# Performance work log

Hardware: AMD Instinct MI355X
Metric: run time of the kernel (lower is better)

The kernel has to match this reference:

```python
import jax, jax.numpy as jnp
import numpy as np

N, E, B = 16384, 65536, 32
D_IN, ED, H, L = 4, 5, 64, 3  # node feat, edge feat, hidden=output, num layers
NEG_SLOPE = 0.1
EPS = 1e-5


def _leaky(v):
    return jnp.where(v > 0, v, NEG_SLOPE * v)


def setup_inputs() -> dict:
    key = jax.random.key(0)
    ks = jax.random.split(key, 32)
    s = 0.05
    inp = {
        'x': jax.random.normal(ks[0], (N, D_IN), jnp.float32),
        'edge_index': jax.random.randint(ks[1], (2, E), 0, N),
        'edge_attr': jax.random.normal(ks[2], (E, ED), jnp.float32),
        'batch': jnp.sort(jax.random.randint(ks[3], (N,), 0, B)),
        # input projection Linear(4 -> H)
        'W_in': s * jax.random.normal(ks[4], (H, D_IN), jnp.float32),
        'b_in': jnp.zeros((H,), jnp.float32),
        # per-layer edge MLP: Linear(ED->H), Linear(H->H), Linear(H->H*H); stacked over L
        'ew1': s * jax.random.normal(ks[5], (L, H, ED), jnp.float32),
        'eb1': jnp.zeros((L, H), jnp.float32),
        'ew2': s * jax.random.normal(ks[6], (L, H, H), jnp.float32),
        'eb2': jnp.zeros((L, H), jnp.float32),
        'ew3': s * jax.random.normal(ks[7], (L, H * H, H), jnp.float32),
        'eb3': jnp.zeros((L, H * H), jnp.float32),
        # NNConv root weight + bias per layer
        'root_w': s * jax.random.normal(ks[8], (L, H, H), jnp.float32),
        'root_b': jnp.zeros((L, H), jnp.float32),
        # LayerNorm per layer
        'ln_g': jnp.ones((L, H), jnp.float32),
        'ln_b': jnp.zeros((L, H), jnp.float32),
        # prediction head: Linear(H->H), Linear(H->H//2), Linear(H//2->1)
        'pw1': s * jax.random.normal(ks[9], (H, H), jnp.float32),
        'pb1': jnp.zeros((H,), jnp.float32),
        'pw2': s * jax.random.normal(ks[10], (H // 2, H), jnp.float32),
        'pb2': jnp.zeros((H // 2,), jnp.float32),
        'pw3': s * jax.random.normal(ks[11], (1, H // 2), jnp.float32),
        'pb3': jnp.zeros((1,), jnp.float32),
    }
    return inp


def reference(x, edge_index, edge_attr, batch, W_in, b_in, ew1, eb1, ew2, eb2,
              ew3, eb3, root_w, root_b, ln_g, ln_b, pw1, pb1, pw2, pb2, pw3, pb3):
    src, dst = edge_index[0], edge_index[1]
    n_nodes = x.shape[0]
    n_edges = edge_attr.shape[0]
    # in-degree for scatter-mean (PyG yields 0 for isolated nodes)
    deg = jax.ops.segment_sum(jnp.ones((n_edges,), x.dtype), dst, num_segments=n_nodes)
    deg = jnp.maximum(deg, 1.0)[:, None]

    # input projection (dropout = identity in eval)
    h = _leaky(x @ W_in.T + b_in)

    for l in range(L):
        # edge MLP -> per-edge weight matrix [E, H, H]
        e = _leaky(edge_attr @ ew1[l].T + eb1[l])
        e = _leaky(e @ ew2[l].T + eb2[l])
        Wf = (e @ ew3[l].T + eb3[l]).reshape(n_edges, H, H)
        # message = x_src @ W_edge, scatter-mean to dst
        msg = jnp.einsum('ei,eio->eo', h[src], Wf)
        agg = jax.ops.segment_sum(msg, dst, num_segments=n_nodes) / deg
        out = agg + h @ root_w[l].T + root_b[l]
        # LayerNorm (post-norm)
        mu = out.mean(-1, keepdims=True)
        var = ((out - mu) ** 2).mean(-1, keepdims=True)
        out = (out - mu) * jax.lax.rsqrt(var + EPS) * ln_g[l] + ln_b[l]
        # activation + (identity) dropout + residual (in==out for all layers)
        h = _leaky(out) + h

    # global mean pool over graphs
    pooled = jax.ops.segment_sum(h, batch, num_segments=B)
    cnt = jax.ops.segment_sum(jnp.ones((n_nodes,), h.dtype), batch, num_segments=B)
    pooled = pooled / jnp.maximum(cnt, 1.0)[:, None]

    # prediction head
    p = _leaky(pooled @ pw1.T + pb1)
    p = _leaky(p @ pw2.T + pb2)
    pred = (p @ pw3.T + pb3).squeeze(-1)  # [B]
    return pred
```

## Files before the change

kernel.cpp:

```cpp
#include <hip/hip_runtime.h>
#include <hip/hip_bf16.h>

#define N_NODES 16384
#define N_EDGES 65536
#define NB      32
#define H       64
#define NLAYERS 3
#define NEG     0.1f
#define LN_EPS  1e-5f

typedef _Float16 f16;
typedef _Float16 f16x2 __attribute__((ext_vector_type(2)));
typedef _Float16 f16x8 __attribute__((ext_vector_type(8)));
typedef __fp16   hf16x2 __attribute__((ext_vector_type(2)));
typedef float    f32x16 __attribute__((ext_vector_type(16)));

union F16x8 { f16x8 v; f16x2 p[4]; int4 i4; int2 i2[2]; };
union F16x2U { f16x2 h2; hf16x2 raw; unsigned int u; };
union F16U   { f16 h; unsigned short u; };

__device__ __forceinline__ f16x2 pkrtz(float a, float b) {
    F16x2U t; t.raw = __builtin_amdgcn_cvt_pkrtz(a, b); return t.h2;
}
__device__ __forceinline__ float leaky(float v) { return v > 0.f ? v : NEG * v; }

__global__ __launch_bounds__(256) void k_setup(const float* __restrict__ x,
                                               const float* __restrict__ Win,
                                               const float* __restrict__ bin,
                                               const int* __restrict__ dst,
                                               const float* __restrict__ ew3,
                                               const float* __restrict__ eb3,
                                               float* __restrict__ h,
                                               float* __restrict__ deg,
                                               f16* __restrict__ Bp) {
    int bid = blockIdx.x;
    if (bid < 4096) {
        int t = bid * 256 + threadIdx.x;
        int n = t >> 6, j = t & 63;
        const float* xr = x + n * 4;
        const float* wr = Win + j * 4;
        float v = bin[j] + xr[0] * wr[0] + xr[1] * wr[1] + xr[2] * wr[2] + xr[3] * wr[3];
        h[t] = leaky(v);
    } else if (bid < 4352) {
        int e = (bid - 4096) * 256 + threadIdx.x;
        atomicAdd(&deg[dst[e]], 1.0f);
    } else {
        int tg    = (bid - 4352) * 256 + threadIdx.x;
        int lane  = tg & 63;
        int gslot = tg >> 6;
        int l     = gslot / 520;
        int slot  = gslot - l * 520;
        const float* ew3l = ew3 + (size_t)l * 262144;
        const float* eb3l = eb3 + (size_t)l * 4096;
        int i   = slot >> 3;
        int rem = slot & 7;
        int ks  = rem >> 1;
        int oq  = rem & 1;
        int o   = oq * 32 + (lane & 31);
        int k0  = ks * 16 + (lane >> 5) * 8;
        float v[8];
        if (i < 64) {
            const float* s = ew3l + ((size_t)(i * 64 + o)) * 64 + k0;
            float4 a = ((const float4*)s)[0];
            float4 b = ((const float4*)s)[1];
            v[0] = a.x; v[1] = a.y; v[2] = a.z; v[3] = a.w;
            v[4] = b.x; v[5] = b.y; v[6] = b.z; v[7] = b.w;
        } else {
#pragma unroll
            for (int j = 0; j < 8; j++) v[j] = eb3l[(k0 + j) * 64 + o];
        }
        union { int4 i4; f16 a[8]; } out;
#pragma unroll
        for (int j = 0; j < 8; j++) out.a[j] = (f16)v[j];
        *(int4*)(Bp + (size_t)l * 266240 + (size_t)slot * 512 + lane * 8) = out.i4;
    }
}

#define HS_STRIDE 76

__device__ __forceinline__ void loadB8(const f16* __restrict__ Bp, int c, int oq, int lane, F16x8* dstB) {
    const f16* base = Bp + (((size_t)(c * 16 + oq)) << 9) + lane * 8;
#pragma unroll
    for (int di = 0; di < 2; di++)
#pragma unroll
        for (int ks = 0; ks < 4; ks++)
            dstB[di * 4 + ks].i4 = *(const int4*)(base + ((di * 8 + ks * 2) << 9));
}
__device__ __forceinline__ void loadB4(const f16* __restrict__ Bp, int oq, int lane, F16x8* dstB) {
    const f16* base = Bp + (((size_t)(512 + oq)) << 9) + lane * 8;
#pragma unroll
    for (int ks = 0; ks < 4; ks++)
        dstB[ks].i4 = *(const int4*)(base + ((ks * 2) << 9));
}

__device__ __forceinline__ void msg_chunk2(int c, const F16x8* __restrict__ B,
                                           const unsigned short* hp0,
                                           const unsigned short* hp1,
                                           const f16x2 (*e2p)[4][4], f32x16* CC) {
    unsigned int rr0 = *(const unsigned int*)(hp0 + 2 * c);
    unsigned int rr1 = *(const unsigned int*)(hp1 + 2 * c);
    F16x2U h00, h01, h10, h11;
    h00.u = __builtin_amdgcn_perm(rr0, rr0, 0x01000100u);
    h10.u = __builtin_amdgcn_perm(rr0, rr0, 0x03020302u);
    h01.u = __builtin_amdgcn_perm(rr1, rr1, 0x01000100u);
    h11.u = __builtin_amdgcn_perm(rr1, rr1, 0x03020302u);
#pragma unroll
    for (int ks = 0; ks < 4; ks++) {
        F16x8 A00, A01, A10, A11;
#pragma unroll
        for (int r = 0; r < 4; r++) {
            A00.p[r] = h00.h2 * e2p[0][ks][r];
            A01.p[r] = h01.h2 * e2p[1][ks][r];
            A10.p[r] = h10.h2 * e2p[0][ks][r];
            A11.p[r] = h11.h2 * e2p[1][ks][r];
        }
        CC[0] = __builtin_amdgcn_mfma_f32_32x32x16_f16(A00.v, B[0 * 4 + ks].v, CC[0], 0, 0, 0);
        CC[1] = __builtin_amdgcn_mfma_f32_32x32x16_f16(A01.v, B[0 * 4 + ks].v, CC[1], 0, 0, 0);
        CC[2] = __builtin_amdgcn_mfma_f32_32x32x16_f16(A10.v, B[1 * 4 + ks].v, CC[2], 0, 0, 0);
        CC[3] = __builtin_amdgcn_mfma_f32_32x32x16_f16(A11.v, B[1 * 4 + ks].v, CC[3], 0, 0, 0);
    }
}

__global__ __launch_bounds__(256, 2) void k_msg(const float* __restrict__ h,
                                                const float* __restrict__ ea,
                                                const float* __restrict__ w1,
                                                const float* __restrict__ b1,
                                                const float* __restrict__ w2,
                                                const float* __restrict__ b2,
                                                const f16* __restrict__ Bp,
                                                const int* __restrict__ src,
                                                const int* __restrict__ dst,
                                                float* __restrict__ agg) {
    __shared__ __align__(16) unsigned short hsL[128 * HS_STRIDE];
    __shared__ __align__(16) unsigned short e1L[128 * 72];
    __shared__ __align__(16) unsigned short e2L[128 * 72];
    __shared__ float eas[128 * 8];
    __shared__ int dstL[128];

    const int t    = threadIdx.x;
    const int lane = t & 63;
    const int w    = t >> 6;
    const int eh   = w >> 1, oq = w & 1;
    const int m    = lane & 31;
    const int kp   = lane >> 5;
    const int eb   = blockIdx.x * 128;

    for (int idx = t; idx < 640; idx += 256) {
        int r = idx / 5, d = idx - r * 5;
        eas[r * 8 + d] = ea[(size_t)eb * 5 + idx];
    }
    {
        int e    = t >> 1;
        int half = t & 1;
        int nsrc = src[eb + e];
        const float4* hr = (const float4*)(h + (size_t)nsrc * 64 + half * 32);
        unsigned int* hrow = (unsigned int*)hsL + e * (HS_STRIDE / 2) + half * 16;
#pragma unroll
        for (int q = 0; q < 8; q++) {
            float4 v = hr[q];
            F16x2U p0, p1;
            p0.raw = __builtin_amdgcn_cvt_pkrtz(v.x, v.y);
            p1.raw = __builtin_amdgcn_cvt_pkrtz(v.z, v.w);
            hrow[q * 2 + 0] = p0.u;
            hrow[q * 2 + 1] = p1.u;
        }
        if (t < 128) dstL[t] = dst[eb + t];
    }
    __syncthreads();

    {
        int kk = t & 63;
        int eg = t >> 6;
        float w1r[5];
#pragma unroll
        for (int d = 0; d < 5; d++) w1r[d] = w1[kk * 5 + d];
        float b1r = b1[kk];
#pragma unroll 4
        for (int g = 0; g < 32; g++) {
            int row = eg * 32 + g;
            float4 a4 = *(const float4*)(eas + row * 8);
            float a5 = eas[row * 8 + 4];
            float v = b1r + a4.x * w1r[0] + a4.y * w1r[1] + a4.z * w1r[2] + a4.w * w1r[3] + a5 * w1r[4];
            F16U z; z.h = (f16)leaky(v);
            e1L[row * 72 + kk] = z.u;
        }
    }
    __syncthreads();

    {
        F16x8 W2f[4];
#pragma unroll
        for (int ks = 0; ks < 4; ks++) {
            const float* s = w2 + (size_t)(oq * 32 + m) * 64 + ks * 16 + kp * 8;
            float4 a = ((const float4*)s)[0];
            float4 b = ((const float4*)s)[1];
            W2f[ks].p[0] = pkrtz(a.x, a.y);
            W2f[ks].p[1] = pkrtz(a.z, a.w);
            W2f[ks].p[2] = pkrtz(b.x, b.y);
            W2f[ks].p[3] = pkrtz(b.z, b.w);
        }
        float b2r = b2[oq * 32 + m];
#pragma unroll
        for (int tt = 0; tt < 2; tt++) {
            f32x16 C2 = {0,0,0,0,0,0,0,0,0,0,0,0,0,0,0,0};
#pragma unroll
            for (int ks = 0; ks < 4; ks++) {
                F16x8 A;
                A.i4 = *(const int4*)(e1L + (size_t)((eh * 2 + tt) * 32 + m) * 72 + ks * 16 + kp * 8);
                C2 = __builtin_amdgcn_mfma_f32_32x32x16_f16(A.v, W2f[ks].v, C2, 0, 0, 0);
            }
#pragma unroll
            for (int reg = 0; reg < 16; reg++) {
                int r = (reg & 3) + 8 * (reg >> 2) + 4 * kp;
                F16U z; z.h = (f16)leaky(C2[reg] + b2r);
                e2L[((eh * 2 + tt) * 32 + r) * 72 + oq * 32 + m] = z.u;
            }
        }
    }
    __syncthreads();

    f16x2 e2p[2][4][4];
#pragma unroll
    for (int tt = 0; tt < 2; tt++) {
#pragma unroll
        for (int ks = 0; ks < 4; ks++) {
            F16x8 q;
            q.i4 = *(const int4*)(e2L + (size_t)((eh * 2 + tt) * 32 + m) * 72 + ks * 16 + kp * 8);
            e2p[tt][ks][0] = q.p[0]; e2p[tt][ks][1] = q.p[1];
            e2p[tt][ks][2] = q.p[2]; e2p[tt][ks][3] = q.p[3];
        }
    }

    f32x16 CC[4];
#pragma unroll
    for (int q = 0; q < 4; q++)
#pragma unroll
        for (int r = 0; r < 16; r++) CC[q][r] = 0.f;

    const unsigned short* hp0 = hsL + ((eh * 2 + 0) * 32 + m) * HS_STRIDE;
    const unsigned short* hp1 = hsL + ((eh * 2 + 1) * 32 + m) * HS_STRIDE;

    F16x8 B0[8], B1[8];
    loadB8(Bp, 0, oq, lane, B0);
    loadB8(Bp, 1, oq, lane, B1);
    for (int it = 0; it < 15; it++) {
        int c = it * 2;
        msg_chunk2(c,     B0, hp0, hp1, e2p, CC);  loadB8(Bp, c + 2, oq, lane, B0);
        msg_chunk2(c + 1, B1, hp0, hp1, e2p, CC);  loadB8(Bp, c + 3, oq, lane, B1);
    }
    msg_chunk2(30, B0, hp0, hp1, e2p, CC);
    loadB4(Bp, oq, lane, B0);
    msg_chunk2(31, B1, hp0, hp1, e2p, CC);

#pragma unroll
    for (int ks = 0; ks < 4; ks++) {
        int koff = (ks * 16 + kp * 8) * 2;
        const char* r0p = (const char*)hsL + (size_t)((eh * 2 + 0) * 32 + m) * (HS_STRIDE * 2) + koff;
        const char* r1p = (const char*)hsL + (size_t)((eh * 2 + 1) * 32 + m) * (HS_STRIDE * 2) + koff;
        F16x8 A0, A1;
        A0.i2[0] = *(const int2*)(r0p); A0.i2[1] = *(const int2*)(r0p + 8);
        A1.i2[0] = *(const int2*)(r1p); A1.i2[1] = *(const int2*)(r1p + 8);
        CC[0] = __builtin_amdgcn_mfma_f32_32x32x16_f16(A0.v, B0[ks].v, CC[0], 0, 0, 0);
        CC[1] = __builtin_amdgcn_mfma_f32_32x32x16_f16(A1.v, B0[ks].v, CC[1], 0, 0, 0);
    }

    int o = oq * 32 + m;
#pragma unroll
    for (int reg = 0; reg < 16; reg++) {
        int r = (reg & 3) + 8 * (reg >> 2) + 4 * kp;
        atomicAdd(&agg[(size_t)dstL[(eh * 2 + 0) * 32 + r] * 64 + o], CC[0][reg] + CC[2][reg]);
    }
#pragma unroll
    for (int reg = 0; reg < 16; reg++) {
        int r = (reg & 3) + 8 * (reg >> 2) + 4 * kp;
        atomicAdd(&agg[(size_t)dstL[(eh * 2 + 1) * 32 + r] * 64 + o], CC[1][reg] + CC[3][reg]);
    }
}

__global__ __launch_bounds__(256) void k_node(const float* __restrict__ agg,
                                              const float* __restrict__ deg,
                                              const float* __restrict__ rw,
                                              const float* __restrict__ rb,
                                              const float* __restrict__ lg,
                                              const float* __restrict__ lb,
                                              float* __restrict__ h,
                                              const int* __restrict__ batch,
                                              float* __restrict__ pooled,
                                              int last) {
    __shared__ __align__(16) unsigned short hA[64 * 72];
    __shared__ float outL[64][68];
    int t = threadIdx.x;
    int nb = blockIdx.x * 64;
    int lane = t & 63, w = t >> 6;
    int nq = w >> 1, oq = w & 1;
    int m = lane & 31, kp = lane >> 5;

    {
        int r = t >> 2, c0 = (t & 3) * 16;
        const float4* hr = (const float4*)(h + (size_t)(nb + r) * 64 + c0);
        unsigned int* drow = (unsigned int*)hA + r * 36 + c0 / 2;
#pragma unroll
        for (int q = 0; q < 4; q++) {
            float4 v = hr[q];
            F16x2U p0, p1;
            p0.raw = __builtin_amdgcn_cvt_pkrtz(v.x, v.y);
            p1.raw = __builtin_amdgcn_cvt_pkrtz(v.z, v.w);
            drow[q * 2] = p0.u; drow[q * 2 + 1] = p1.u;
        }
    }
    F16x8 Bf[4];
#pragma unroll
    for (int ks = 0; ks < 4; ks++) {
        const float* s = rw + (size_t)(oq * 32 + m) * 64 + ks * 16 + kp * 8;
        float4 a = ((const float4*)s)[0];
        float4 b = ((const float4*)s)[1];
        Bf[ks].p[0] = pkrtz(a.x, a.y);
        Bf[ks].p[1] = pkrtz(a.z, a.w);
        Bf[ks].p[2] = pkrtz(b.x, b.y);
        Bf[ks].p[3] = pkrtz(b.z, b.w);
    }
    __syncthreads();

    f32x16 C = {0,0,0,0,0,0,0,0,0,0,0,0,0,0,0,0};
#pragma unroll
    for (int ks = 0; ks < 4; ks++) {
        F16x8 A;
        A.i4 = *(const int4*)(hA + (size_t)(nq * 32 + m) * 72 + ks * 16 + kp * 8);
        C = __builtin_amdgcn_mfma_f32_32x32x16_f16(A.v, Bf[ks].v, C, 0, 0, 0);
    }

    int o = oq * 32 + m;
#pragma unroll
    for (int reg = 0; reg < 16; reg++) {
        int r = (reg & 3) + 8 * (reg >> 2) + 4 * kp;
        int n = nq * 32 + r;
        outL[n][o] = C[reg] + rb[o] + agg[(size_t)(nb + n) * 64 + o] / fmaxf(deg[nb + n], 1.0f);
    }
    __syncthreads();

    float gj = lg[lane], bj = lb[lane];
    float accp = 0.f;
    int cur = batch[nb + w * 16];
    for (int q = 0; q < 16; q++) {
        int n = w * 16 + q;
        float v = outL[n][lane];
        float mu = v;
#pragma unroll
        for (int msk = 32; msk > 0; msk >>= 1) mu += __shfl_xor(mu, msk);
        mu *= (1.f / 64.f);
        float d = v - mu;
        float var = d * d;
#pragma unroll
        for (int msk = 32; msk > 0; msk >>= 1) var += __shfl_xor(var, msk);
        var *= (1.f / 64.f);
        float ov = d * rsqrtf(var + LN_EPS) * gj + bj;
        float hn = leaky(ov) + h[(size_t)(nb + n) * 64 + lane];
        h[(size_t)(nb + n) * 64 + lane] = hn;
        if (last) {
            int b = batch[nb + n];
            if (b != cur) { atomicAdd(&pooled[cur * 64 + lane], accp); accp = 0.f; cur = b; }
            accp += hn;
        }
    }
    if (last) atomicAdd(&pooled[cur * 64 + lane], accp);
}

__global__ __launch_bounds__(256) void k_head(const float* __restrict__ pooled,
                                              const int* __restrict__ batch,
                                              const float* __restrict__ pw1, const float* __restrict__ pb1,
                                              const float* __restrict__ pw2, const float* __restrict__ pb2,
                                              const float* __restrict__ pw3, const float* __restrict__ pb3,
                                              float* __restrict__ out) {
    __shared__ float cntL[32];
    __shared__ float ps[32][64];
    __shared__ float p1[32][64];
    __shared__ float p2[32][32];
    int t = threadIdx.x;
    if (t < 32) cntL[t] = 0.f;
    __syncthreads();
    {
        const int4* bp4 = (const int4*)(batch + t * 64);
        int cur = batch[t * 64];
        float c = 0.f;
        for (int q = 0; q < 16; q++) {
            int4 b4 = bp4[q];
            int bs[4] = { b4.x, b4.y, b4.z, b4.w };
#pragma unroll
            for (int e = 0; e < 4; e++) {
                if (bs[e] != cur) { atomicAdd(&cntL[cur], c); cur = bs[e]; c = 0.f; }
                c += 1.f;
            }
        }
        atomicAdd(&cntL[cur], c);
    }
    __syncthreads();
    for (int idx = t; idx < 2048; idx += 256) {
        int b = idx >> 6, j = idx & 63;
        ps[b][j] = pooled[idx] / fmaxf(cntL[b], 1.0f);
    }
    __syncthreads();
    for (int idx = t; idx < 2048; idx += 256) {
        int b = idx >> 6, j = idx & 63;
        float v = pb1[j];
#pragma unroll 8
        for (int i = 0; i < 64; i++) v += ps[b][i] * pw1[j * 64 + i];
        p1[b][j] = leaky(v);
    }
    __syncthreads();
    for (int idx = t; idx < 1024; idx += 256) {
        int b = idx >> 5, j = idx & 31;
        float v = pb2[j];
#pragma unroll 8
        for (int i = 0; i < 64; i++) v += p1[b][i] * pw2[j * 64 + i];
        p2[b][j] = leaky(v);
    }
    __syncthreads();
    if (t < 32) {
        float v = pb3[0];
#pragma unroll 8
        for (int i = 0; i < 32; i++) v += p2[t][i] * pw3[i];
        out[t] = v;
    }
}

extern "C" void kernel_launch(void* const* d_in, const int* in_sizes, int n_in,
                              void* d_out, int out_size, void* d_ws, size_t ws_size,
                              hipStream_t stream) {
    const float* x    = (const float*)d_in[0];
    const int*   eidx = (const int*)  d_in[1];
    const float* ea   = (const float*)d_in[2];
    const int*   bat  = (const int*)  d_in[3];
    const float* Win  = (const float*)d_in[4];
    const float* bin  = (const float*)d_in[5];
    const float* ew1  = (const float*)d_in[6];
    const float* eb1  = (const float*)d_in[7];
    const float* ew2  = (const float*)d_in[8];
    const float* eb2  = (const float*)d_in[9];
    const float* ew3  = (const float*)d_in[10];
    const float* eb3  = (const float*)d_in[11];
    const float* rw   = (const float*)d_in[12];
    const float* rb   = (const float*)d_in[13];
    const float* lg   = (const float*)d_in[14];
    const float* lb   = (const float*)d_in[15];
    const float* pw1  = (const float*)d_in[16];
    const float* pb1  = (const float*)d_in[17];
    const float* pw2  = (const float*)d_in[18];
    const float* pb2  = (const float*)d_in[19];
    const float* pw3  = (const float*)d_in[20];
    const float* pb3  = (const float*)d_in[21];
    float* out = (float*)d_out;

    float* ws     = (float*)d_ws;
    float* h      = ws;
    float* agg    = ws + 1048576;
    float* deg    = ws + 4194304;
    float* pooled = ws + 4210688;
    f16*   Bp     = (f16*)(ws + 4212800);

    const int* srcp = eidx;
    const int* dstp = eidx + N_EDGES;

    (void)hipMemsetAsync(agg, 0, (size_t)3164224 * sizeof(float), stream);

    k_setup<<<4742, 256, 0, stream>>>(x, Win, bin, dstp, ew3, eb3, h, deg, Bp);

    for (int l = 0; l < NLAYERS; l++) {
        float* agg_l = agg + (size_t)l * N_NODES * H;
        k_msg <<<N_EDGES / 128, 256, 0, stream>>>(h, ea, ew1 + l * 320, eb1 + l * 64,
                                                  ew2 + l * 4096, eb2 + l * 64,
                                                  Bp + (size_t)l * 266240,
                                                  srcp, dstp, agg_l);
        k_node<<<N_NODES / 64, 256, 0, stream>>>(agg_l, deg, rw + l * 4096, rb + l * 64,
                                                 lg + l * 64, lb + l * 64, h,
                                                 bat, pooled, l == NLAYERS - 1 ? 1 : 0);
    }

    k_head<<<1, 256, 0, stream>>>(pooled, bat, pw1, pb1, pw2, pb2, pw3, pb3, out);
}
```

Measured before the change: 323.1 us.

## Remap message MFMA so each wave owns one edge tile and all outputs

The work split across the four waves of the message kernel changes. Before, each wave handled two 32-edge tiles for one half of the output columns. Now each wave handles one 32-edge tile for all 64 output columns, so each A operand (h times e2) is built once and reused across two B tiles. This halves the per-wave register copy of e2 and the VALU work spent forming A fragments. In exchange each wave loads twice as many B fragments per chunk (16 vs 8 int4 loads), which raises per-wave global/L2 traffic for the packed weight matrix and increases VGPR pressure for the B double buffer.

```diff
diff --git a/kernel.cpp b/kernel.cpp
--- a/kernel.cpp
+++ b/kernel.cpp
@@ -78,46 +78,38 @@
 
 #define HS_STRIDE 76
 
-__device__ __forceinline__ void loadB8(const f16* __restrict__ Bp, int c, int oq, int lane, F16x8* dstB) {
-    const f16* base = Bp + (((size_t)(c * 16 + oq)) << 9) + lane * 8;
-#pragma unroll
-    for (int di = 0; di < 2; di++)
-#pragma unroll
-        for (int ks = 0; ks < 4; ks++)
-            dstB[di * 4 + ks].i4 = *(const int4*)(base + ((di * 8 + ks * 2) << 9));
-}
-__device__ __forceinline__ void loadB4(const f16* __restrict__ Bp, int oq, int lane, F16x8* dstB) {
-    const f16* base = Bp + (((size_t)(512 + oq)) << 9) + lane * 8;
-#pragma unroll
-    for (int ks = 0; ks < 4; ks++)
-        dstB[ks].i4 = *(const int4*)(base + ((ks * 2) << 9));
-}
-
-__device__ __forceinline__ void msg_chunk2(int c, const F16x8* __restrict__ B,
-                                           const unsigned short* hp0,
-                                           const unsigned short* hp1,
-                                           const f16x2 (*e2p)[4][4], f32x16* CC) {
-    unsigned int rr0 = *(const unsigned int*)(hp0 + 2 * c);
-    unsigned int rr1 = *(const unsigned int*)(hp1 + 2 * c);
-    F16x2U h00, h01, h10, h11;
-    h00.u = __builtin_amdgcn_perm(rr0, rr0, 0x01000100u);
-    h10.u = __builtin_amdgcn_perm(rr0, rr0, 0x03020302u);
-    h01.u = __builtin_amdgcn_perm(rr1, rr1, 0x01000100u);
-    h11.u = __builtin_amdgcn_perm(rr1, rr1, 0x03020302u);
+__device__ __forceinline__ void loadB16(const f16* __restrict__ Bp, int c, int lane, F16x8* dstB) {
+    const f16* base = Bp + (((size_t)(c * 16)) << 9) + lane * 8;
+#pragma unroll
+    for (int s = 0; s < 16; s++)
+        dstB[s].i4 = *(const int4*)(base + (s << 9));
+}
+__device__ __forceinline__ void loadBias8(const f16* __restrict__ Bp, int lane, F16x8* dstB) {
+    const f16* base = Bp + (((size_t)512) << 9) + lane * 8;
+#pragma unroll
+    for (int s = 0; s < 8; s++)
+        dstB[s].i4 = *(const int4*)(base + (s << 9));
+}
+
+__device__ __forceinline__ void msg_chunk(int c, const F16x8* __restrict__ B,
+                                          const unsigned short* hp,
+                                          const f16x2 (*e2p)[4], f32x16* CC) {
+    unsigned int rr = *(const unsigned int*)(hp + 2 * c);
+    F16x2U h0, h1;
+    h0.u = __builtin_amdgcn_perm(rr, rr, 0x01000100u);
+    h1.u = __builtin_amdgcn_perm(rr, rr, 0x03020302u);
 #pragma unroll
     for (int ks = 0; ks < 4; ks++) {
-        F16x8 A00, A01, A10, A11;
+        F16x8 A0, A1;
 #pragma unroll
         for (int r = 0; r < 4; r++) {
-            A00.p[r] = h00.h2 * e2p[0][ks][r];
-            A01.p[r] = h01.h2 * e2p[1][ks][r];
-            A10.p[r] = h10.h2 * e2p[0][ks][r];
-            A11.p[r] = h11.h2 * e2p[1][ks][r];
-        }
-        CC[0] = __builtin_amdgcn_mfma_f32_32x32x16_f16(A00.v, B[0 * 4 + ks].v, CC[0], 0, 0, 0);
-        CC[1] = __builtin_amdgcn_mfma_f32_32x32x16_f16(A01.v, B[0 * 4 + ks].v, CC[1], 0, 0, 0);
-        CC[2] = __builtin_amdgcn_mfma_f32_32x32x16_f16(A10.v, B[1 * 4 + ks].v, CC[2], 0, 0, 0);
-        CC[3] = __builtin_amdgcn_mfma_f32_32x32x16_f16(A11.v, B[1 * 4 + ks].v, CC[3], 0, 0, 0);
+            A0.p[r] = h0.h2 * e2p[ks][r];
+            A1.p[r] = h1.h2 * e2p[ks][r];
+        }
+        CC[0] = __builtin_amdgcn_mfma_f32_32x32x16_f16(A0.v, B[ks * 2 + 0].v, CC[0], 0, 0, 0);
+        CC[1] = __builtin_amdgcn_mfma_f32_32x32x16_f16(A0.v, B[ks * 2 + 1].v, CC[1], 0, 0, 0);
+        CC[2] = __builtin_amdgcn_mfma_f32_32x32x16_f16(A1.v, B[8 + ks * 2 + 0].v, CC[2], 0, 0, 0);
+        CC[3] = __builtin_amdgcn_mfma_f32_32x32x16_f16(A1.v, B[8 + ks * 2 + 1].v, CC[3], 0, 0, 0);
     }
 }
 
@@ -219,16 +211,14 @@
     }
     __syncthreads();
 
-    f16x2 e2p[2][4][4];
-#pragma unroll
-    for (int tt = 0; tt < 2; tt++) {
-#pragma unroll
-        for (int ks = 0; ks < 4; ks++) {
-            F16x8 q;
-            q.i4 = *(const int4*)(e2L + (size_t)((eh * 2 + tt) * 32 + m) * 72 + ks * 16 + kp * 8);
-            e2p[tt][ks][0] = q.p[0]; e2p[tt][ks][1] = q.p[1];
-            e2p[tt][ks][2] = q.p[2]; e2p[tt][ks][3] = q.p[3];
-        }
+    const int tt = w;
+    f16x2 e2p[4][4];
+#pragma unroll
+    for (int ks = 0; ks < 4; ks++) {
+        F16x8 q;
+        q.i4 = *(const int4*)(e2L + (size_t)(tt * 32 + m) * 72 + ks * 16 + kp * 8);
+        e2p[ks][0] = q.p[0]; e2p[ks][1] = q.p[1];
+        e2p[ks][2] = q.p[2]; e2p[ks][3] = q.p[3];
     }
 
     f32x16 CC[4];
@@ -237,43 +227,36 @@
 #pragma unroll
         for (int r = 0; r < 16; r++) CC[q][r] = 0.f;
 
-    const unsigned short* hp0 = hsL + ((eh * 2 + 0) * 32 + m) * HS_STRIDE;
-    const unsigned short* hp1 = hsL + ((eh * 2 + 1) * 32 + m) * HS_STRIDE;
-
-    F16x8 B0[8], B1[8];
-    loadB8(Bp, 0, oq, lane, B0);
-    loadB8(Bp, 1, oq, lane, B1);
+    const unsigned short* hp = hsL + (tt * 32 + m) * HS_STRIDE;
+
+    F16x8 B0[16], B1[16];
+    loadB16(Bp, 0, lane, B0);
+    loadB16(Bp, 1, lane, B1);
     for (int it = 0; it < 15; it++) {
         int c = it * 2;
-        msg_chunk2(c,     B0, hp0, hp1, e2p, CC);  loadB8(Bp, c + 2, oq, lane, B0);
-        msg_chunk2(c + 1, B1, hp0, hp1, e2p, CC);  loadB8(Bp, c + 3, oq, lane, B1);
-    }
-    msg_chunk2(30, B0, hp0, hp1, e2p, CC);
-    loadB4(Bp, oq, lane, B0);
-    msg_chunk2(31, B1, hp0, hp1, e2p, CC);
+        msg_chunk(c,     B0, hp, e2p, CC);  loadB16(Bp, c + 2, lane, B0);
+        msg_chunk(c + 1, B1, hp, e2p, CC);  loadB16(Bp, c + 3, lane, B1);
+    }
+    msg_chunk(30, B0, hp, e2p, CC);
+    loadBias8(Bp, lane, B0);
+    msg_chunk(31, B1, hp, e2p, CC);
 
 #pragma unroll
     for (int ks = 0; ks < 4; ks++) {
         int koff = (ks * 16 + kp * 8) * 2;
-        const char* r0p = (const char*)hsL + (size_t)((eh * 2 + 0) * 32 + m) * (HS_STRIDE * 2) + koff;
-        const char* r1p = (const char*)hsL + (size_t)((eh * 2 + 1) * 32 + m) * (HS_STRIDE * 2) + koff;
-        F16x8 A0, A1;
-        A0.i2[0] = *(const int2*)(r0p); A0.i2[1] = *(const int2*)(r0p + 8);
-        A1.i2[0] = *(const int2*)(r1p); A1.i2[1] = *(const int2*)(r1p + 8);
-        CC[0] = __builtin_amdgcn_mfma_f32_32x32x16_f16(A0.v, B0[ks].v, CC[0], 0, 0, 0);
-        CC[1] = __builtin_amdgcn_mfma_f32_32x32x16_f16(A1.v, B0[ks].v, CC[1], 0, 0, 0);
-    }
-
-    int o = oq * 32 + m;
+        const char* rp = (const char*)hsL + (size_t)(tt * 32 + m) * (HS_STRIDE * 2) + koff;
+        F16x8 A;
+        A.i2[0] = *(const int2*)(rp); A.i2[1] = *(const int2*)(rp + 8);
+        CC[0] = __builtin_amdgcn_mfma_f32_32x32x16_f16(A.v, B0[ks * 2 + 0].v, CC[0], 0, 0, 0);
+        CC[1] = __builtin_amdgcn_mfma_f32_32x32x16_f16(A.v, B0[ks * 2 + 1].v, CC[1], 0, 0, 0);
+    }
+
 #pragma unroll
     for (int reg = 0; reg < 16; reg++) {
         int r = (reg & 3) + 8 * (reg >> 2) + 4 * kp;
-        atomicAdd(&agg[(size_t)dstL[(eh * 2 + 0) * 32 + r] * 64 + o], CC[0][reg] + CC[2][reg]);
-    }
-#pragma unroll
-    for (int reg = 0; reg < 16; reg++) {
-        int r = (reg & 3) + 8 * (reg >> 2) + 4 * kp;
-        atomicAdd(&agg[(size_t)dstL[(eh * 2 + 1) * 32 + r] * 64 + o], CC[1][reg] + CC[3][reg]);
+        float* basep = &agg[(size_t)dstL[tt * 32 + r] * 64];
+        atomicAdd(basep + m,      CC[0][reg] + CC[2][reg]);
+        atomicAdd(basep + 32 + m, CC[1][reg] + CC[3][reg]);
     }
 }
 
```

After: 550.9 us. 1.7x slower.

## Stage per-chunk B weights through LDS with async global_load_lds double buffering

Applied to the files above, without the earlier changes.

Replaces the per-wave direct global loads of the packed edge-weight B fragments with a cooperative double-buffered LDS staging scheme. Each wave issues global_load_lds for a quarter of the chunk, so the two oq waves sharing the same B data no longer fetch it twice from global memory. e1L and e2L are merged into one buffer to free LDS for the two 16KB stage buffers. The cost is explicit barriers and full vmcnt waits every chunk, which serialize the pipeline, and higher LDS use that may lower occupancy below the two blocks per CU set by launch bounds.

```diff
diff --git a/kernel.cpp b/kernel.cpp
--- a/kernel.cpp
+++ b/kernel.cpp
@@ -78,19 +78,22 @@
 
 #define HS_STRIDE 76
 
-__device__ __forceinline__ void loadB8(const f16* __restrict__ Bp, int c, int oq, int lane, F16x8* dstB) {
-    const f16* base = Bp + (((size_t)(c * 16 + oq)) << 9) + lane * 8;
+__device__ __forceinline__ void stageChunk(const f16* __restrict__ Bp, int c, f16* P, int w, int lane) {
+    const f16* g = Bp + (((size_t)(c * 16 + w * 4)) << 9) + lane * 8;
+    f16* l = P + ((w * 4) << 9);
+#pragma unroll
+    for (int s = 0; s < 4; s++)
+        __builtin_amdgcn_global_load_lds(
+            (const __attribute__((address_space(1))) unsigned int*)(g + (s << 9)),
+            (__attribute__((address_space(3))) unsigned int*)(l + (s << 9)), 16, 0, 0);
+}
+
+__device__ __forceinline__ void readB(const f16* P, int oq, int lane, F16x8* Bf) {
 #pragma unroll
     for (int di = 0; di < 2; di++)
 #pragma unroll
         for (int ks = 0; ks < 4; ks++)
-            dstB[di * 4 + ks].i4 = *(const int4*)(base + ((di * 8 + ks * 2) << 9));
-}
-__device__ __forceinline__ void loadB4(const f16* __restrict__ Bp, int oq, int lane, F16x8* dstB) {
-    const f16* base = Bp + (((size_t)(512 + oq)) << 9) + lane * 8;
-#pragma unroll
-    for (int ks = 0; ks < 4; ks++)
-        dstB[ks].i4 = *(const int4*)(base + ((ks * 2) << 9));
+            Bf[di * 4 + ks].i4 = *(const int4*)(P + ((di * 8 + ks * 2 + oq) << 9) + lane * 8);
 }
 
 __device__ __forceinline__ void msg_chunk2(int c, const F16x8* __restrict__ B,
@@ -132,8 +135,9 @@
                                                 const int* __restrict__ dst,
                                                 float* __restrict__ agg) {
     __shared__ __align__(16) unsigned short hsL[128 * HS_STRIDE];
-    __shared__ __align__(16) unsigned short e1L[128 * 72];
-    __shared__ __align__(16) unsigned short e2L[128 * 72];
+    __shared__ __align__(16) unsigned short eL[128 * 72];
+    __shared__ __align__(16) f16 Pb0[8192];
+    __shared__ __align__(16) f16 Pb1[8192];
     __shared__ float eas[128 * 8];
     __shared__ int dstL[128];
 
@@ -182,7 +186,7 @@
             float a5 = eas[row * 8 + 4];
             float v = b1r + a4.x * w1r[0] + a4.y * w1r[1] + a4.z * w1r[2] + a4.w * w1r[3] + a5 * w1r[4];
             F16U z; z.h = (f16)leaky(v);
-            e1L[row * 72 + kk] = z.u;
+            eL[row * 72 + kk] = z.u;
         }
     }
     __syncthreads();
@@ -200,20 +204,24 @@
             W2f[ks].p[3] = pkrtz(b.z, b.w);
         }
         float b2r = b2[oq * 32 + m];
+        F16x8 A8[8];
+#pragma unroll
+        for (int tt = 0; tt < 2; tt++)
+#pragma unroll
+            for (int ks = 0; ks < 4; ks++)
+                A8[tt * 4 + ks].i4 = *(const int4*)(eL + (size_t)((eh * 2 + tt) * 32 + m) * 72 + ks * 16 + kp * 8);
+        __syncthreads();
 #pragma unroll
         for (int tt = 0; tt < 2; tt++) {
             f32x16 C2 = {0,0,0,0,0,0,0,0,0,0,0,0,0,0,0,0};
 #pragma unroll
-            for (int ks = 0; ks < 4; ks++) {
-                F16x8 A;
-                A.i4 = *(const int4*)(e1L + (size_t)((eh * 2 + tt) * 32 + m) * 72 + ks * 16 + kp * 8);
-                C2 = __builtin_amdgcn_mfma_f32_32x32x16_f16(A.v, W2f[ks].v, C2, 0, 0, 0);
-            }
+            for (int ks = 0; ks < 4; ks++)
+                C2 = __builtin_amdgcn_mfma_f32_32x32x16_f16(A8[tt * 4 + ks].v, W2f[ks].v, C2, 0, 0, 0);
 #pragma unroll
             for (int reg = 0; reg < 16; reg++) {
                 int r = (reg & 3) + 8 * (reg >> 2) + 4 * kp;
                 F16U z; z.h = (f16)leaky(C2[reg] + b2r);
-                e2L[((eh * 2 + tt) * 32 + r) * 72 + oq * 32 + m] = z.u;
+                eL[((eh * 2 + tt) * 32 + r) * 72 + oq * 32 + m] = z.u;
             }
         }
     }
@@ -225,7 +233,7 @@
 #pragma unroll
         for (int ks = 0; ks < 4; ks++) {
             F16x8 q;
-            q.i4 = *(const int4*)(e2L + (size_t)((eh * 2 + tt) * 32 + m) * 72 + ks * 16 + kp * 8);
+            q.i4 = *(const int4*)(eL + (size_t)((eh * 2 + tt) * 32 + m) * 72 + ks * 16 + kp * 8);
             e2p[tt][ks][0] = q.p[0]; e2p[tt][ks][1] = q.p[1];
             e2p[tt][ks][2] = q.p[2]; e2p[tt][ks][3] = q.p[3];
         }
@@ -240,18 +248,36 @@
     const unsigned short* hp0 = hsL + ((eh * 2 + 0) * 32 + m) * HS_STRIDE;
     const unsigned short* hp1 = hsL + ((eh * 2 + 1) * 32 + m) * HS_STRIDE;
 
-    F16x8 B0[8], B1[8];
-    loadB8(Bp, 0, oq, lane, B0);
-    loadB8(Bp, 1, oq, lane, B1);
-    for (int it = 0; it < 15; it++) {
-        int c = it * 2;
-        msg_chunk2(c,     B0, hp0, hp1, e2p, CC);  loadB8(Bp, c + 2, oq, lane, B0);
-        msg_chunk2(c + 1, B1, hp0, hp1, e2p, CC);  loadB8(Bp, c + 3, oq, lane, B1);
-    }
-    msg_chunk2(30, B0, hp0, hp1, e2p, CC);
-    loadB4(Bp, oq, lane, B0);
-    msg_chunk2(31, B1, hp0, hp1, e2p, CC);
-
+    F16x8 BfA[8], BfB[8];
+    stageChunk(Bp, 0, Pb0, w, lane);
+    stageChunk(Bp, 1, Pb1, w, lane);
+    asm volatile("s_waitcnt vmcnt(0)" ::: "memory");
+    __builtin_amdgcn_s_barrier();
+    readB(Pb0, oq, lane, BfA);
+    asm volatile("s_waitcnt lgkmcnt(0)" ::: "memory");
+    __builtin_amdgcn_s_barrier();
+
+#pragma unroll 1
+    for (int j = 0; j < 15; j++) {
+        readB(Pb1, oq, lane, BfB);
+        stageChunk(Bp, 2 * j + 2, Pb0, w, lane);
+        msg_chunk2(2 * j, BfA, hp0, hp1, e2p, CC);
+        asm volatile("s_waitcnt vmcnt(0) lgkmcnt(0)" ::: "memory");
+        __builtin_amdgcn_s_barrier();
+        readB(Pb0, oq, lane, BfA);
+        stageChunk(Bp, 2 * j + 3, Pb1, w, lane);
+        msg_chunk2(2 * j + 1, BfB, hp0, hp1, e2p, CC);
+        asm volatile("s_waitcnt vmcnt(0) lgkmcnt(0)" ::: "memory");
+        __builtin_amdgcn_s_barrier();
+    }
+    readB(Pb1, oq, lane, BfB);
+    msg_chunk2(30, BfA, hp0, hp1, e2p, CC);
+    msg_chunk2(31, BfB, hp0, hp1, e2p, CC);
+
+    F16x8 Bb[4];
+#pragma unroll
+    for (int ks = 0; ks < 4; ks++)
+        Bb[ks].i4 = *(const int4*)(Bp + (((size_t)(512 + ks * 2 + oq)) << 9) + lane * 8);
 #pragma unroll
     for (int ks = 0; ks < 4; ks++) {
         int koff = (ks * 16 + kp * 8) * 2;
@@ -260,8 +286,8 @@
         F16x8 A0, A1;
         A0.i2[0] = *(const int2*)(r0p); A0.i2[1] = *(const int2*)(r0p + 8);
         A1.i2[0] = *(const int2*)(r1p); A1.i2[1] = *(const int2*)(r1p + 8);
-        CC[0] = __builtin_amdgcn_mfma_f32_32x32x16_f16(A0.v, B0[ks].v, CC[0], 0, 0, 0);
-        CC[1] = __builtin_amdgcn_mfma_f32_32x32x16_f16(A1.v, B0[ks].v, CC[1], 0, 0, 0);
+        CC[0] = __builtin_amdgcn_mfma_f32_32x32x16_f16(A0.v, Bb[ks].v, CC[0], 0, 0, 0);
+        CC[1] = __builtin_amdgcn_mfma_f32_32x32x16_f16(A1.v, Bb[ks].v, CC[1], 0, 0, 0);
     }
 
     int o = oq * 32 + m;
```

After: 323.9 us. Within noise of the previous version (+0.2%).
